# Performance work log

Measured on AMD Instinct MI355X. Metric: run time of the kernel, lower is better.

## Reference

```python
import math
import jax, jax.numpy as jnp
import numpy as np

H = 1024          # hidden size
NH = 16           # num attention heads
HD = H // NH      # head dim = 64
MAXPOS = 1024
HYP_W = 0.5


def setup_inputs() -> dict:
    key = jax.random.key(0)
    ks = jax.random.split(key, 9)
    B, S = 4, 1024
    scale = 1.0 / math.sqrt(H)
    return {
        "hidden_states": jax.random.normal(ks[0], (B, S, H), jnp.float32),
        "attention_mask": jnp.zeros((B, 1, 1, S), jnp.float32),
        "hyperbolic_attention_scores": jax.random.normal(ks[1], (B, S, S), jnp.float32),
        "Wq": jax.random.normal(ks[2], (H, H), jnp.float32) * scale,
        "bq": jnp.zeros((H,), jnp.float32),
        "Wk": jax.random.normal(ks[3], (H, H), jnp.float32) * scale,
        "bk": jnp.zeros((H,), jnp.float32),
        "Wv": jax.random.normal(ks[4], (H, H), jnp.float32) * scale,
        "bv": jnp.zeros((H,), jnp.float32),
        "dist_emb": jax.random.normal(ks[5], (2 * MAXPOS - 1, HD), jnp.float32) * 0.02,
    }


def reference(hidden_states, attention_mask, hyperbolic_attention_scores,
              Wq, bq, Wk, bk, Wv, bv, dist_emb):
    B, S, _ = hidden_states.shape

    def split_heads(x):  # [B,S,H] -> [B,NH,S,HD]
        return x.reshape(B, S, NH, HD).transpose(0, 2, 1, 3)

    q = split_heads(hidden_states @ Wq + bq)
    k = split_heads(hidden_states @ Wk + bk)
    v = split_heads(hidden_states @ Wv + bv)

    # raw scores [B,NH,Sq,Sk]
    scores = jnp.einsum("bhqd,bhkd->bhqk", q, k)

    # relative_key_query position bias
    distance = jnp.arange(S)[:, None] - jnp.arange(S)[None, :]  # [Sq,Sk]
    pe = dist_emb[distance + MAXPOS - 1]                        # [Sq,Sk,HD]
    scores = scores + jnp.einsum("bhld,lrd->bhlr", q, pe)
    scores = scores + jnp.einsum("bhrd,lrd->bhlr", k, pe)

    scores = scores / math.sqrt(HD)
    scores = scores + HYP_W * hyperbolic_attention_scores[:, None, :, :]
    scores = scores + attention_mask

    probs = jax.nn.softmax(scores, axis=-1)
    ctx = jnp.einsum("bhqk,bhkd->bhqd", probs, v)  # [B,NH,S,HD]
    ctx = ctx.transpose(0, 2, 1, 3).reshape(B, S, H)
    return ctx
```

## Files before the change

### kernel.cpp

```cpp
#include <hip/hip_runtime.h>
#include <math.h>

#define S_SEQ 1024
#define NHEAD 16
#define HDIM  64
#define BATCH 4

typedef __attribute__((ext_vector_type(8))) short bf16x8;
typedef __attribute__((ext_vector_type(4))) float f32x4;

#define MFMA16 __builtin_amdgcn_mfma_f32_16x16x32_bf16

__device__ __forceinline__ float bf2f(unsigned short h) {
    union { unsigned u; float f; } un; un.u = ((unsigned)h) << 16; return un.f;
}
__device__ __forceinline__ unsigned short f2bf(float x) {
    union { float f; unsigned u; } un; un.f = x;
    unsigned r = un.u + 0x7FFFu + ((un.u >> 16) & 1u);
    return (unsigned short)(r >> 16);
}
__device__ __forceinline__ unsigned pack2bf(float a, float b) {
    return (unsigned)f2bf(a) | ((unsigned)f2bf(b) << 16);
}
__device__ __forceinline__ void glds16(const unsigned short* g, unsigned short* l) {
    __builtin_amdgcn_global_load_lds(
        (const __attribute__((address_space(1))) void*)g,
        (__attribute__((address_space(3))) void*)l, 16, 0, 0);
}

#define HS_F4 1048576
#define PE_F4 32752
__global__ __launch_bounds__(256) void conv_kernel(
    const float* __restrict__ hs, const float* __restrict__ de,
    unsigned short* __restrict__ hsb, unsigned short* __restrict__ peb)
{
    int i = blockIdx.x * 256 + threadIdx.x;
    if (i < HS_F4) {
        float4 v = ((const float4*)hs)[i];
        uint2 o;
        o.x = pack2bf(v.x, v.y);
        o.y = pack2bf(v.z, v.w);
        *(uint2*)(hsb + 4 * (size_t)i) = o;
    } else if (i < HS_F4 + PE_F4) {
        int j = i - HS_F4;
        float4 v = ((const float4*)de)[j];
        uint2 o;
        o.x = pack2bf(v.x, v.y);
        o.y = pack2bf(v.z, v.w);
        *(uint2*)(peb + 4 * (size_t)j) = o;
    }
}

__global__ __launch_bounds__(256) void wtrans_kernel(
    const float* __restrict__ Wq, const float* __restrict__ Wk,
    const float* __restrict__ Wv, unsigned short* __restrict__ wt)
{
    __shared__ float tl[64 * 67];
    const int which = blockIdx.z;
    const float* W = (which == 0) ? Wq : (which == 1) ? Wk : Wv;
    unsigned short* out = wt + (size_t)which * 1024 * 1024;
    const int k0 = blockIdx.x * 64, n0 = blockIdx.y * 64;
    const int t = threadIdx.x;

#pragma unroll
    for (int it = 0; it < 4; ++it) {
        int idx = t + it * 256;
        int kr = idx >> 4;
        int c4 = (idx & 15) << 2;
        float4 v = *(const float4*)(W + (size_t)(k0 + kr) * 1024 + n0 + c4);
        tl[kr * 67 + c4 + 0] = v.x; tl[kr * 67 + c4 + 1] = v.y;
        tl[kr * 67 + c4 + 2] = v.z; tl[kr * 67 + c4 + 3] = v.w;
    }
    __syncthreads();
#pragma unroll
    for (int it = 0; it < 2; ++it) {
        int idx = t + it * 256;
        int nr = idx >> 3;
        int k8 = (idx & 7) << 3;
        unsigned short r[8];
#pragma unroll
        for (int e = 0; e < 8; ++e) r[e] = f2bf(tl[(k8 + e) * 67 + nr]);
        uint4 o;
        o.x = (unsigned)r[0] | ((unsigned)r[1] << 16);
        o.y = (unsigned)r[2] | ((unsigned)r[3] << 16);
        o.z = (unsigned)r[4] | ((unsigned)r[5] << 16);
        o.w = (unsigned)r[6] | ((unsigned)r[7] << 16);
        *(uint4*)(out + (size_t)(n0 + nr) * 1024 + k0 + k8) = o;
    }
}

__global__ __launch_bounds__(256, 3) void qkv_mfma_kernel(
    const unsigned short* __restrict__ hsb, const unsigned short* __restrict__ wt,
    const float* __restrict__ bq, const float* __restrict__ bk,
    const float* __restrict__ bv,
    unsigned short* __restrict__ qo, unsigned short* __restrict__ ko,
    unsigned short* __restrict__ vo)
{
    __shared__ unsigned short As[128 * 64];
    __shared__ unsigned short Bs[128 * 64];

    const int t = threadIdx.x;
    const int lane = t & 63, w = t >> 6;
    const int l16 = lane & 15, quad = lane >> 4;
    const int wm = w >> 1, wn = w & 1;
    const int lrow = lane >> 3, cs = lane & 7;
    const int n0 = blockIdx.x * 128, m0 = blockIdx.y * 128;
    const int which = blockIdx.z;
    const unsigned short* wts = wt + (size_t)which * 1024 * 1024;
    const float* bias = (which == 0) ? bq : (which == 1) ? bk : bv;

    f32x4 acc[4][4];
#pragma unroll
    for (int i = 0; i < 4; ++i)
#pragma unroll
        for (int j = 0; j < 4; ++j) acc[i][j] = (f32x4){0.f, 0.f, 0.f, 0.f};

    for (int kk = 0; kk < 1024; kk += 64) {
#pragma unroll
        for (int it = 0; it < 4; ++it) {
            int mrow = 32 * w + 8 * it + lrow;
            int kch = cs ^ (mrow & 7);
            glds16(hsb + (size_t)(m0 + mrow) * 1024 + kk + kch * 8,
                   &As[(32 * w + 8 * it) * 64]);
            glds16(wts + (size_t)(n0 + mrow) * 1024 + kk + kch * 8,
                   &Bs[(32 * w + 8 * it) * 64]);
        }
        __syncthreads();

        bf16x8 af[4][2], bf[4][2];
#pragma unroll
        for (int i = 0; i < 4; ++i) {
            int am = 64 * wm + 16 * i + l16;
            int base = am * 64;
            af[i][0] = *(bf16x8*)&As[base + ((quad ^ (am & 7)) << 3)];
            af[i][1] = *(bf16x8*)&As[base + (((quad + 4) ^ (am & 7)) << 3)];
        }
#pragma unroll
        for (int j = 0; j < 4; ++j) {
            int bn = 64 * wn + 16 * j + l16;
            int base = bn * 64;
            bf[j][0] = *(bf16x8*)&Bs[base + ((quad ^ (bn & 7)) << 3)];
            bf[j][1] = *(bf16x8*)&Bs[base + (((quad + 4) ^ (bn & 7)) << 3)];
        }
#pragma unroll
        for (int i = 0; i < 4; ++i)
#pragma unroll
            for (int j = 0; j < 4; ++j) {
                acc[i][j] = MFMA16(af[i][0], bf[j][0], acc[i][j], 0, 0, 0);
                acc[i][j] = MFMA16(af[i][1], bf[j][1], acc[i][j], 0, 0, 0);
            }
        __syncthreads();
    }

#pragma unroll
    for (int j = 0; j < 4; ++j) {
        int n = n0 + 64 * wn + 16 * j + l16;
        float bvv = bias[n];
        int hh = n >> 6, hd = n & 63;
#pragma unroll
        for (int i = 0; i < 4; ++i) {
            int mb = m0 + 64 * wm + 16 * i + 4 * quad;
            int bb = mb >> 10, s = mb & 1023;
            if (which == 2) {
                uint2 o;
                o.x = pack2bf(acc[i][j][0] + bvv, acc[i][j][1] + bvv);
                o.y = pack2bf(acc[i][j][2] + bvv, acc[i][j][3] + bvv);
                *(uint2*)(vo + ((size_t)(bb * NHEAD + hh) * HDIM + hd) * S_SEQ + s) = o;
            } else {
                unsigned short* out = (which == 0) ? qo : ko;
#pragma unroll
                for (int r = 0; r < 4; ++r)
                    out[((size_t)(bb * NHEAD + hh) * S_SEQ + s + r) * HDIM + hd] =
                        f2bf(acc[i][j][r] + bvv);
            }
        }
    }
}

__global__ __launch_bounds__(256, 4) void attn_mfma_kernel(
    const unsigned short* __restrict__ qw, const unsigned short* __restrict__ kw,
    const unsigned short* __restrict__ vtw, const unsigned short* __restrict__ peb,
    const float* __restrict__ hyp, const float* __restrict__ mask,
    float* __restrict__ out)
{
    __shared__ unsigned short pes[96 * 64];
    __shared__ unsigned short QDs[64 * 100];
    __shared__ unsigned short KDs[96 * 36];
    __shared__ unsigned short ps[64 * 32];

    const int t = threadIdx.x;
    const int lane = t & 63, w = t >> 6;
    const int l16 = lane & 15, quad = lane >> 4;
    const int lL = 16 * w + l16;
    const int l0 = blockIdx.x * 64;
    const int h = blockIdx.y, b = blockIdx.z;

    const unsigned short* qb = qw + ((size_t)(b * NHEAD + h) * S_SEQ + l0) * HDIM;
    const unsigned short* kb = kw + (size_t)(b * NHEAD + h) * S_SEQ * HDIM;
    const unsigned short* vtb = vtw + (size_t)(b * NHEAD + h) * HDIM * S_SEQ;
    const float* hypb = hyp + (size_t)b * S_SEQ * S_SEQ + (size_t)(l0 + lL) * S_SEQ;
    const float* maskb = mask + b * S_SEQ;

    const bf16x8 qf0 = *(const bf16x8*)(qb + lL * 64 + quad * 8);
    const bf16x8 qf1 = *(const bf16x8*)(qb + lL * 64 + 32 + quad * 8);

    const int pb0 = l0 + 992;
    int sb = pb0 % 96;
    int cQ = (pb0 - lL) % 96;

    const int strow = t >> 3, stp = t & 7;
    const int swzl = (lL >> 1) & 3;

    f32x4 accO[4];
#pragma unroll
    for (int jf = 0; jf < 4; ++jf) accO[jf] = (f32x4){0.f, 0.f, 0.f, 0.f};
    float m_run = -INFINITY, lsum = 0.f;

#pragma unroll
    for (int it = 0; it < 2; ++it) {
        int idx = t + it * 256;
        int row = idx >> 3, p = idx & 7;
        int ar = pb0 + 32 + row;
        int slot = ar % 96;
        int src = ar > 2046 ? 2046 : ar;
        *(uint4*)&pes[slot * 64 + (p << 3)] =
            *(const uint4*)(peb + (size_t)src * 64 + ((p ^ (slot & 7)) << 3));
    }
    __syncthreads();

#pragma unroll
    for (int jd = 0; jd < 4; ++jd) {
        int s = sb + 32 + 16 * jd + l16; if (s >= 96) s -= 96;
        const int sw = s & 7;
        bf16x8 p0 = *(bf16x8*)&pes[s * 64 + ((quad ^ sw) << 3)];
        bf16x8 p1 = *(bf16x8*)&pes[s * 64 + (((quad + 4) ^ sw) << 3)];
        f32x4 aq = (f32x4){0.f, 0.f, 0.f, 0.f};
        aq = MFMA16(p0, qf0, aq, 0, 0, 0);
        aq = MFMA16(p1, qf1, aq, 0, 0, 0);
        int cb = cQ + 32 + 16 * jd + 4 * quad;
#pragma unroll
        for (int i = 0; i < 4; ++i) {
            int c = cb + i; if (c >= 96) c -= 96;
            QDs[lL * 100 + c] = f2bf(aq[i]);
        }
    }

    bf16x8 kf00 = *(const bf16x8*)(kb + (size_t)l16 * 64 + quad * 8);
    bf16x8 kf01 = *(const bf16x8*)(kb + (size_t)l16 * 64 + 32 + quad * 8);
    bf16x8 kf10 = *(const bf16x8*)(kb + (size_t)(16 + l16) * 64 + quad * 8);
    bf16x8 kf11 = *(const bf16x8*)(kb + (size_t)(16 + l16) * 64 + 32 + quad * 8);
    uint4 peReg;
    {
        int slot = sb + strow; if (slot >= 96) slot -= 96;
        peReg = *(const uint4*)(peb + (size_t)(pb0 + strow) * 64 +
                                ((stp ^ (slot & 7)) << 3));
    }

    const int fstart = (w < 2) ? 3 * w : 2 * w + 2;
    const int fcnt   = (w < 2) ? 3 : 2;

    for (int kt = 0; kt < 32; ++kt) {
        const int r0 = 32 * kt;

        const float4 hv0 = *(const float4*)(hypb + r0 + 4 * quad);
        const float4 hv1 = *(const float4*)(hypb + r0 + 16 + 4 * quad);
        const float4 mv0 = *(const float4*)(maskb + r0 + 4 * quad);
        const float4 mv1 = *(const float4*)(maskb + r0 + 16 + 4 * quad);

        {
            int slot = sb + strow; if (slot >= 96) slot -= 96;
            *(uint4*)&pes[slot * 64 + (stp << 3)] = peReg;
        }
        __syncthreads();

        f32x4 accS0 = (f32x4){0.f, 0.f, 0.f, 0.f};
        f32x4 accS1 = (f32x4){0.f, 0.f, 0.f, 0.f};
        accS0 = MFMA16(kf00, qf0, accS0, 0, 0, 0);
        accS0 = MFMA16(kf01, qf1, accS0, 0, 0, 0);
        accS1 = MFMA16(kf10, qf0, accS1, 0, 0, 0);
        accS1 = MFMA16(kf11, qf1, accS1, 0, 0, 0);

#pragma unroll
        for (int jd = 0; jd < 2; ++jd) {
            int s = sb + 16 * jd + l16; if (s >= 96) s -= 96;
            const int sw = s & 7;
            bf16x8 p0 = *(bf16x8*)&pes[s * 64 + ((quad ^ sw) << 3)];
            bf16x8 p1 = *(bf16x8*)&pes[s * 64 + (((quad + 4) ^ sw) << 3)];
            f32x4 aq = (f32x4){0.f, 0.f, 0.f, 0.f};
            aq = MFMA16(p0, qf0, aq, 0, 0, 0);
            aq = MFMA16(p1, qf1, aq, 0, 0, 0);
            int cb = cQ + 16 * jd + 4 * quad;
#pragma unroll
            for (int i = 0; i < 4; ++i) {
                int c = cb + i; if (c >= 96) c -= 96;
                QDs[lL * 100 + c] = f2bf(aq[i]);
            }
        }

#pragma unroll
        for (int jk = 0; jk < 3; ++jk) {
            if (jk < fcnt) {
                const int f = fstart + jk;
                const int diB = 16 * ((f + 1) >> 1);
                const int rB = (f & 1) ? 0 : 16;
                int s = sb + diB + l16; if (s >= 96) s -= 96;
                const int sw = s & 7;
                bf16x8 p0 = *(bf16x8*)&pes[s * 64 + ((quad ^ sw) << 3)];
                bf16x8 p1 = *(bf16x8*)&pes[s * 64 + (((quad + 4) ^ sw) << 3)];
                f32x4 ak = (f32x4){0.f, 0.f, 0.f, 0.f};
                if (rB == 0) {
                    ak = MFMA16(p0, kf00, ak, 0, 0, 0);
                    ak = MFMA16(p1, kf01, ak, 0, 0, 0);
                } else {
                    ak = MFMA16(p0, kf10, ak, 0, 0, 0);
                    ak = MFMA16(p1, kf11, ak, 0, 0, 0);
                }
                const int colr = rB + l16;
                const int aB = diB + colr + 4 * quad - 16;
#pragma unroll
                for (int i = 0; i < 4; ++i)
                    KDs[(aB + i) * 36 + colr] = f2bf(ak[i]);
            }
        }
        __syncthreads();

        {
            const int r0n = (kt < 31) ? r0 + 32 : r0;
            kf00 = *(const bf16x8*)(kb + (size_t)(r0n + l16) * 64 + quad * 8);
            kf01 = *(const bf16x8*)(kb + (size_t)(r0n + l16) * 64 + 32 + quad * 8);
            kf10 = *(const bf16x8*)(kb + (size_t)(r0n + 16 + l16) * 64 + quad * 8);
            kf11 = *(const bf16x8*)(kb + (size_t)(r0n + 16 + l16) * 64 + 32 + quad * 8);
            int sbn = sb, pbn = pb0 - r0n;
            if (kt < 31) { sbn = sb - 32; if (sbn < 0) sbn += 96; }
            int slotN = sbn + strow; if (slotN >= 96) slotN -= 96;
            peReg = *(const uint4*)(peb + (size_t)(pbn + strow) * 64 +
                                    ((stp ^ (slotN & 7)) << 3));
        }
        bf16x8 vvA[4];
#pragma unroll
        for (int jf = 0; jf < 4; ++jf)
            vvA[jf] = *(const bf16x8*)(vtb + (size_t)(16 * jf + l16) * S_SEQ +
                                       r0 + quad * 8);

        float sc0[4], sc1[4];
        {
            uint2 qd2 = *(uint2*)&QDs[lL * 100 + sb + 28 - 4 * quad];
            uint2 kd2 = *(uint2*)&KDs[(lL + 15) * 36 + 4 * quad];
            sc0[0] = (accS0[0] + bf2f((unsigned short)(qd2.y >> 16)) +
                      bf2f((unsigned short)(kd2.x & 0xffff))) * 0.125f + 0.5f * hv0.x + mv0.x;
            sc0[1] = (accS0[1] + bf2f((unsigned short)(qd2.y & 0xffff)) +
                      bf2f((unsigned short)(kd2.x >> 16))) * 0.125f + 0.5f * hv0.y + mv0.y;
            sc0[2] = (accS0[2] + bf2f((unsigned short)(qd2.x >> 16)) +
                      bf2f((unsigned short)(kd2.y & 0xffff))) * 0.125f + 0.5f * hv0.z + mv0.z;
            sc0[3] = (accS0[3] + bf2f((unsigned short)(qd2.x & 0xffff)) +
                      bf2f((unsigned short)(kd2.y >> 16))) * 0.125f + 0.5f * hv0.w + mv0.w;
        }
        {
            uint2 qd2 = *(uint2*)&QDs[lL * 100 + sb + 12 - 4 * quad];
            uint2 kd2 = *(uint2*)&KDs[(lL + 15) * 36 + 16 + 4 * quad];
            sc1[0] = (accS1[0] + bf2f((unsigned short)(qd2.y >> 16)) +
                      bf2f((unsigned short)(kd2.x & 0xffff))) * 0.125f + 0.5f * hv1.x + mv1.x;
            sc1[1] = (accS1[1] + bf2f((unsigned short)(qd2.y & 0xffff)) +
                      bf2f((unsigned short)(kd2.x >> 16))) * 0.125f + 0.5f * hv1.y + mv1.y;
            sc1[2] = (accS1[2] + bf2f((unsigned short)(qd2.x >> 16)) +
                      bf2f((unsigned short)(kd2.y & 0xffff))) * 0.125f + 0.5f * hv1.z + mv1.z;
            sc1[3] = (accS1[3] + bf2f((unsigned short)(qd2.x & 0xffff)) +
                      bf2f((unsigned short)(kd2.y >> 16))) * 0.125f + 0.5f * hv1.w + mv1.w;
        }

        float mx = fmaxf(fmaxf(fmaxf(sc0[0], sc0[1]), fmaxf(sc0[2], sc0[3])),
                         fmaxf(fmaxf(sc1[0], sc1[1]), fmaxf(sc1[2], sc1[3])));
        mx = fmaxf(mx, __shfl_xor(mx, 16));
        mx = fmaxf(mx, __shfl_xor(mx, 32));
        const float m_new = fmaxf(m_run, mx);
        const float al = __expf(m_run - m_new);
        m_run = m_new;
        float rs = 0.f;
#pragma unroll
        for (int i = 0; i < 4; ++i) { sc0[i] = __expf(sc0[i] - m_new); rs += sc0[i]; }
#pragma unroll
        for (int i = 0; i < 4; ++i) { sc1[i] = __expf(sc1[i] - m_new); rs += sc1[i]; }
        rs += __shfl_xor(rs, 16);
        rs += __shfl_xor(rs, 32);
        lsum = lsum * al + rs;

        {
            uint2 pw;
            pw.x = pack2bf(sc0[0], sc0[1]); pw.y = pack2bf(sc0[2], sc0[3]);
            *(uint2*)&ps[lL * 32 + (((quad >> 1) ^ swzl) << 3) + 4 * (quad & 1)] = pw;
            pw.x = pack2bf(sc1[0], sc1[1]); pw.y = pack2bf(sc1[2], sc1[3]);
            *(uint2*)&ps[lL * 32 + (((2 + (quad >> 1)) ^ swzl) << 3) + 4 * (quad & 1)] = pw;
        }

        const bf16x8 pf = *(const bf16x8*)&ps[lL * 32 + ((quad ^ swzl) << 3)];
        const float alv0 = __shfl(al, 4 * quad + 0);
        const float alv1 = __shfl(al, 4 * quad + 1);
        const float alv2 = __shfl(al, 4 * quad + 2);
        const float alv3 = __shfl(al, 4 * quad + 3);
#pragma unroll
        for (int jf = 0; jf < 4; ++jf) {
            f32x4 o = accO[jf];
            o[0] *= alv0; o[1] *= alv1; o[2] *= alv2; o[3] *= alv3;
            o = MFMA16(pf, vvA[jf], o, 0, 0, 0);
            accO[jf] = o;
        }

        sb -= 32; if (sb < 0) sb += 96;
        cQ -= 32; if (cQ < 0) cQ += 96;
    }

    const float ls0 = __shfl(lsum, 4 * quad + 0);
    const float ls1 = __shfl(lsum, 4 * quad + 1);
    const float ls2 = __shfl(lsum, 4 * quad + 2);
    const float ls3 = __shfl(lsum, 4 * quad + 3);
#pragma unroll
    for (int jf = 0; jf < 4; ++jf) {
        const size_t col = (size_t)h * 64 + 16 * jf + l16;
        float* ob = out + ((size_t)b * S_SEQ + l0 + 16 * w + 4 * quad) * 1024 + col;
        ob[0]        = accO[jf][0] / ls0;
        ob[1024]     = accO[jf][1] / ls1;
        ob[2048]     = accO[jf][2] / ls2;
        ob[3072]     = accO[jf][3] / ls3;
    }
}

extern "C" void kernel_launch(void* const* d_in, const int* in_sizes, int n_in,
                              void* d_out, int out_size, void* d_ws, size_t ws_size,
                              hipStream_t stream) {
    const float* hs   = (const float*)d_in[0];
    const float* mask = (const float*)d_in[1];
    const float* hyp  = (const float*)d_in[2];
    const float* Wq   = (const float*)d_in[3];
    const float* bq   = (const float*)d_in[4];
    const float* Wk   = (const float*)d_in[5];
    const float* bk   = (const float*)d_in[6];
    const float* Wv   = (const float*)d_in[7];
    const float* bv   = (const float*)d_in[8];
    const float* de   = (const float*)d_in[9];

    char* ws = (char*)d_ws;
    unsigned short* qw  = (unsigned short*)(ws);
    unsigned short* kw  = (unsigned short*)(ws + (8u << 20));
    unsigned short* vtw = (unsigned short*)(ws + (16u << 20));
    unsigned short* hsb = (unsigned short*)(ws + (24u << 20));
    unsigned short* wt  = (unsigned short*)(ws + (32u << 20));
    unsigned short* peb = (unsigned short*)(ws + (38u << 20));

    conv_kernel<<<dim3((HS_F4 + PE_F4 + 255) / 256), 256, 0, stream>>>(hs, de, hsb, peb);
    wtrans_kernel<<<dim3(16, 16, 3), 256, 0, stream>>>(Wq, Wk, Wv, wt);
    qkv_mfma_kernel<<<dim3(8, 32, 3), 256, 0, stream>>>(hsb, wt, bq, bk, bv, qw, kw, vtw);
    attn_mfma_kernel<<<dim3(16, NHEAD, BATCH), 256, 0, stream>>>(
        qw, kw, vtw, peb, hyp, mask, (float*)d_out);
}
```

Before: 298.0 us.

## Software-pipeline K-position bias via double-buffered KDs and merge prep kernels

The attention loop now computes the key-position-bias tile for the next iteration after the PV MFMA, writing into a double-buffered KDs array, and the PE ring grows from 96 to 160 rows so the data needed ahead of time is resident. This leaves one __syncthreads per iteration instead of two, and the global loads for the next K fragments and PE row are issued at the top of the iteration. In exchange, the larger shared memory and register footprint lowers the launch bound from 4 to 3 blocks per CU. Separately, the bf16 conversion and weight-transpose kernels are merged into one launch to save a kernel launch.

```diff
diff --git a/kernel.cpp b/kernel.cpp
--- a/kernel.cpp
+++ b/kernel.cpp
@@ -30,37 +30,44 @@
 
 #define HS_F4 1048576
 #define PE_F4 32752
-__global__ __launch_bounds__(256) void conv_kernel(
+#define CONV_BLKS ((HS_F4 + PE_F4 + 255) / 256)
+
+__global__ __launch_bounds__(256) void prep_kernel(
     const float* __restrict__ hs, const float* __restrict__ de,
-    unsigned short* __restrict__ hsb, unsigned short* __restrict__ peb)
-{
-    int i = blockIdx.x * 256 + threadIdx.x;
-    if (i < HS_F4) {
-        float4 v = ((const float4*)hs)[i];
-        uint2 o;
-        o.x = pack2bf(v.x, v.y);
-        o.y = pack2bf(v.z, v.w);
-        *(uint2*)(hsb + 4 * (size_t)i) = o;
-    } else if (i < HS_F4 + PE_F4) {
-        int j = i - HS_F4;
-        float4 v = ((const float4*)de)[j];
-        uint2 o;
-        o.x = pack2bf(v.x, v.y);
-        o.y = pack2bf(v.z, v.w);
-        *(uint2*)(peb + 4 * (size_t)j) = o;
-    }
-}
-
-__global__ __launch_bounds__(256) void wtrans_kernel(
     const float* __restrict__ Wq, const float* __restrict__ Wk,
-    const float* __restrict__ Wv, unsigned short* __restrict__ wt)
+    const float* __restrict__ Wv,
+    unsigned short* __restrict__ hsb, unsigned short* __restrict__ peb,
+    unsigned short* __restrict__ wt)
 {
     __shared__ float tl[64 * 67];
-    const int which = blockIdx.z;
+    const int bx = blockIdx.x;
+    const int t = threadIdx.x;
+
+    if (bx < CONV_BLKS) {
+        int i = bx * 256 + t;
+        if (i < HS_F4) {
+            float4 v = ((const float4*)hs)[i];
+            uint2 o;
+            o.x = pack2bf(v.x, v.y);
+            o.y = pack2bf(v.z, v.w);
+            *(uint2*)(hsb + 4 * (size_t)i) = o;
+        } else if (i < HS_F4 + PE_F4) {
+            int j = i - HS_F4;
+            float4 v = ((const float4*)de)[j];
+            uint2 o;
+            o.x = pack2bf(v.x, v.y);
+            o.y = pack2bf(v.z, v.w);
+            *(uint2*)(peb + 4 * (size_t)j) = o;
+        }
+        return;
+    }
+
+    const int id = bx - CONV_BLKS;
+    const int which = id >> 8;
+    const int rem = id & 255;
     const float* W = (which == 0) ? Wq : (which == 1) ? Wk : Wv;
-    unsigned short* out = wt + (size_t)which * 1024 * 1024;
-    const int k0 = blockIdx.x * 64, n0 = blockIdx.y * 64;
-    const int t = threadIdx.x;
+    unsigned short* outp = wt + (size_t)which * 1024 * 1024;
+    const int k0 = (rem >> 4) * 64, n0 = (rem & 15) * 64;
 
 #pragma unroll
     for (int it = 0; it < 4; ++it) {
@@ -85,7 +92,7 @@
         o.y = (unsigned)r[2] | ((unsigned)r[3] << 16);
         o.z = (unsigned)r[4] | ((unsigned)r[5] << 16);
         o.w = (unsigned)r[6] | ((unsigned)r[7] << 16);
-        *(uint4*)(out + (size_t)(n0 + nr) * 1024 + k0 + k8) = o;
+        *(uint4*)(outp + (size_t)(n0 + nr) * 1024 + k0 + k8) = o;
     }
 }
 
@@ -167,25 +174,25 @@
                 o.y = pack2bf(acc[i][j][2] + bvv, acc[i][j][3] + bvv);
                 *(uint2*)(vo + ((size_t)(bb * NHEAD + hh) * HDIM + hd) * S_SEQ + s) = o;
             } else {
-                unsigned short* out = (which == 0) ? qo : ko;
+                unsigned short* outp = (which == 0) ? qo : ko;
 #pragma unroll
                 for (int r = 0; r < 4; ++r)
-                    out[((size_t)(bb * NHEAD + hh) * S_SEQ + s + r) * HDIM + hd] =
+                    outp[((size_t)(bb * NHEAD + hh) * S_SEQ + s + r) * HDIM + hd] =
                         f2bf(acc[i][j][r] + bvv);
             }
         }
     }
 }
 
-__global__ __launch_bounds__(256, 4) void attn_mfma_kernel(
+__global__ __launch_bounds__(256, 3) void attn_mfma_kernel(
     const unsigned short* __restrict__ qw, const unsigned short* __restrict__ kw,
     const unsigned short* __restrict__ vtw, const unsigned short* __restrict__ peb,
     const float* __restrict__ hyp, const float* __restrict__ mask,
     float* __restrict__ out)
 {
-    __shared__ unsigned short pes[96 * 64];
+    __shared__ unsigned short pes[160 * 64];
     __shared__ unsigned short QDs[64 * 100];
-    __shared__ unsigned short KDs[96 * 36];
+    __shared__ unsigned short KDs[2][96 * 36];
     __shared__ unsigned short ps[64 * 32];
 
     const int t = threadIdx.x;
@@ -205,23 +212,37 @@
     const bf16x8 qf1 = *(const bf16x8*)(qb + lL * 64 + 32 + quad * 8);
 
     const int pb0 = l0 + 992;
-    int sb = pb0 % 96;
+    int sbP = pb0 % 160;
+    int sbQ = pb0 % 96;
     int cQ = (pb0 - lL) % 96;
 
     const int strow = t >> 3, stp = t & 7;
     const int swzl = (lL >> 1) & 3;
 
+    const int fstart = (w < 2) ? 3 * w : 2 * w + 2;
+    const int fcnt   = (w < 2) ? 3 : 2;
+
     f32x4 accO[4];
 #pragma unroll
     for (int jf = 0; jf < 4; ++jf) accO[jf] = (f32x4){0.f, 0.f, 0.f, 0.f};
     float m_run = -INFINITY, lsum = 0.f;
 
-#pragma unroll
-    for (int it = 0; it < 2; ++it) {
+    bf16x8 kfC0 = *(const bf16x8*)(kb + (size_t)l16 * 64 + quad * 8);
+    bf16x8 kfC1 = *(const bf16x8*)(kb + (size_t)l16 * 64 + 32 + quad * 8);
+    bf16x8 kfC2 = *(const bf16x8*)(kb + (size_t)(16 + l16) * 64 + quad * 8);
+    bf16x8 kfC3 = *(const bf16x8*)(kb + (size_t)(16 + l16) * 64 + 32 + quad * 8);
+    uint4 peReg;
+    {
+        int ar = pb0 - 64 + strow;
+        peReg = *(const uint4*)(peb + (size_t)ar * 64 + ((stp ^ (ar & 7)) << 3));
+    }
+
+#pragma unroll
+    for (int it = 0; it < 4; ++it) {
         int idx = t + it * 256;
         int row = idx >> 3, p = idx & 7;
-        int ar = pb0 + 32 + row;
-        int slot = ar % 96;
+        int ar = pb0 - 32 + row;
+        int slot = ar % 160;
         int src = ar > 2046 ? 2046 : ar;
         *(uint4*)&pes[slot * 64 + (p << 3)] =
             *(const uint4*)(peb + (size_t)src * 64 + ((p ^ (slot & 7)) << 3));
@@ -230,7 +251,7 @@
 
 #pragma unroll
     for (int jd = 0; jd < 4; ++jd) {
-        int s = sb + 32 + 16 * jd + l16; if (s >= 96) s -= 96;
+        int s = sbP + 32 + 16 * jd + l16; if (s >= 160) s -= 160;
         const int sw = s & 7;
         bf16x8 p0 = *(bf16x8*)&pes[s * 64 + ((quad ^ sw) << 3)];
         bf16x8 p1 = *(bf16x8*)&pes[s * 64 + (((quad + 4) ^ sw) << 3)];
@@ -245,44 +266,76 @@
         }
     }
 
-    bf16x8 kf00 = *(const bf16x8*)(kb + (size_t)l16 * 64 + quad * 8);
-    bf16x8 kf01 = *(const bf16x8*)(kb + (size_t)l16 * 64 + 32 + quad * 8);
-    bf16x8 kf10 = *(const bf16x8*)(kb + (size_t)(16 + l16) * 64 + quad * 8);
-    bf16x8 kf11 = *(const bf16x8*)(kb + (size_t)(16 + l16) * 64 + 32 + quad * 8);
-    uint4 peReg;
     {
-        int slot = sb + strow; if (slot >= 96) slot -= 96;
-        peReg = *(const uint4*)(peb + (size_t)(pb0 + strow) * 64 +
-                                ((stp ^ (slot & 7)) << 3));
-    }
-
-    const int fstart = (w < 2) ? 3 * w : 2 * w + 2;
-    const int fcnt   = (w < 2) ? 3 : 2;
+        unsigned short* kdp = KDs[0];
+#pragma unroll
+        for (int jk = 0; jk < 3; ++jk) {
+            if (jk < fcnt) {
+                const int f = fstart + jk;
+                const int diB = 16 * ((f + 1) >> 1);
+                const int rB = (f & 1) ? 0 : 16;
+                int s = sbP + diB + l16; if (s >= 160) s -= 160;
+                const int sw = s & 7;
+                bf16x8 p0 = *(bf16x8*)&pes[s * 64 + ((quad ^ sw) << 3)];
+                bf16x8 p1 = *(bf16x8*)&pes[s * 64 + (((quad + 4) ^ sw) << 3)];
+                f32x4 ak = (f32x4){0.f, 0.f, 0.f, 0.f};
+                if (rB == 0) {
+                    ak = MFMA16(p0, kfC0, ak, 0, 0, 0);
+                    ak = MFMA16(p1, kfC1, ak, 0, 0, 0);
+                } else {
+                    ak = MFMA16(p0, kfC2, ak, 0, 0, 0);
+                    ak = MFMA16(p1, kfC3, ak, 0, 0, 0);
+                }
+                const int colr = rB + l16;
+                const int aB = diB + colr + 4 * quad - 16;
+#pragma unroll
+                for (int i = 0; i < 4; ++i)
+                    kdp[(aB + i) * 36 + colr] = f2bf(ak[i]);
+            }
+        }
+    }
 
     for (int kt = 0; kt < 32; ++kt) {
         const int r0 = 32 * kt;
+        __syncthreads();
 
         const float4 hv0 = *(const float4*)(hypb + r0 + 4 * quad);
         const float4 hv1 = *(const float4*)(hypb + r0 + 16 + 4 * quad);
         const float4 mv0 = *(const float4*)(maskb + r0 + 4 * quad);
         const float4 mv1 = *(const float4*)(maskb + r0 + 16 + 4 * quad);
-
+        bf16x8 vvA[4];
+#pragma unroll
+        for (int jf = 0; jf < 4; ++jf)
+            vvA[jf] = *(const bf16x8*)(vtb + (size_t)(16 * jf + l16) * S_SEQ +
+                                       r0 + quad * 8);
+        const int r0n = (kt < 31) ? r0 + 32 : r0;
+        bf16x8 kfN0 = *(const bf16x8*)(kb + (size_t)(r0n + l16) * 64 + quad * 8);
+        bf16x8 kfN1 = *(const bf16x8*)(kb + (size_t)(r0n + l16) * 64 + 32 + quad * 8);
+        bf16x8 kfN2 = *(const bf16x8*)(kb + (size_t)(r0n + 16 + l16) * 64 + quad * 8);
+        bf16x8 kfN3 = *(const bf16x8*)(kb + (size_t)(r0n + 16 + l16) * 64 + 32 + quad * 8);
+        uint4 peRegN;
         {
-            int slot = sb + strow; if (slot >= 96) slot -= 96;
+            int ar = pb0 - r0 - 96 + strow;
+            int src = ar < 0 ? 0 : ar;
+            peRegN = *(const uint4*)(peb + (size_t)src * 64 + ((stp ^ (ar & 7)) << 3));
+        }
+
+        {
+            int sbS = sbP - 64; if (sbS < 0) sbS += 160;
+            int slot = sbS + strow; if (slot >= 160) slot -= 160;
             *(uint4*)&pes[slot * 64 + (stp << 3)] = peReg;
         }
-        __syncthreads();
 
         f32x4 accS0 = (f32x4){0.f, 0.f, 0.f, 0.f};
         f32x4 accS1 = (f32x4){0.f, 0.f, 0.f, 0.f};
-        accS0 = MFMA16(kf00, qf0, accS0, 0, 0, 0);
-        accS0 = MFMA16(kf01, qf1, accS0, 0, 0, 0);
-        accS1 = MFMA16(kf10, qf0, accS1, 0, 0, 0);
-        accS1 = MFMA16(kf11, qf1, accS1, 0, 0, 0);
+        accS0 = MFMA16(kfC0, qf0, accS0, 0, 0, 0);
+        accS0 = MFMA16(kfC1, qf1, accS0, 0, 0, 0);
+        accS1 = MFMA16(kfC2, qf0, accS1, 0, 0, 0);
+        accS1 = MFMA16(kfC3, qf1, accS1, 0, 0, 0);
 
 #pragma unroll
         for (int jd = 0; jd < 2; ++jd) {
-            int s = sb + 16 * jd + l16; if (s >= 96) s -= 96;
+            int s = sbP + 16 * jd + l16; if (s >= 160) s -= 160;
             const int sw = s & 7;
             bf16x8 p0 = *(bf16x8*)&pes[s * 64 + ((quad ^ sw) << 3)];
             bf16x8 p1 = *(bf16x8*)&pes[s * 64 + (((quad + 4) ^ sw) << 3)];
@@ -297,55 +350,11 @@
             }
         }
 
-#pragma unroll
-        for (int jk = 0; jk < 3; ++jk) {
-            if (jk < fcnt) {
-                const int f = fstart + jk;
-                const int diB = 16 * ((f + 1) >> 1);
-                const int rB = (f & 1) ? 0 : 16;
-                int s = sb + diB + l16; if (s >= 96) s -= 96;
-                const int sw = s & 7;
-                bf16x8 p0 = *(bf16x8*)&pes[s * 64 + ((quad ^ sw) << 3)];
-                bf16x8 p1 = *(bf16x8*)&pes[s * 64 + (((quad + 4) ^ sw) << 3)];
-                f32x4 ak = (f32x4){0.f, 0.f, 0.f, 0.f};
-                if (rB == 0) {
-                    ak = MFMA16(p0, kf00, ak, 0, 0, 0);
-                    ak = MFMA16(p1, kf01, ak, 0, 0, 0);
-                } else {
-                    ak = MFMA16(p0, kf10, ak, 0, 0, 0);
-                    ak = MFMA16(p1, kf11, ak, 0, 0, 0);
-                }
-                const int colr = rB + l16;
-                const int aB = diB + colr + 4 * quad - 16;
-#pragma unroll
-                for (int i = 0; i < 4; ++i)
-                    KDs[(aB + i) * 36 + colr] = f2bf(ak[i]);
-            }
-        }
-        __syncthreads();
-
-        {
-            const int r0n = (kt < 31) ? r0 + 32 : r0;
-            kf00 = *(const bf16x8*)(kb + (size_t)(r0n + l16) * 64 + quad * 8);
-            kf01 = *(const bf16x8*)(kb + (size_t)(r0n + l16) * 64 + 32 + quad * 8);
-            kf10 = *(const bf16x8*)(kb + (size_t)(r0n + 16 + l16) * 64 + quad * 8);
-            kf11 = *(const bf16x8*)(kb + (size_t)(r0n + 16 + l16) * 64 + 32 + quad * 8);
-            int sbn = sb, pbn = pb0 - r0n;
-            if (kt < 31) { sbn = sb - 32; if (sbn < 0) sbn += 96; }
-            int slotN = sbn + strow; if (slotN >= 96) slotN -= 96;
-            peReg = *(const uint4*)(peb + (size_t)(pbn + strow) * 64 +
-                                    ((stp ^ (slotN & 7)) << 3));
-        }
-        bf16x8 vvA[4];
-#pragma unroll
-        for (int jf = 0; jf < 4; ++jf)
-            vvA[jf] = *(const bf16x8*)(vtb + (size_t)(16 * jf + l16) * S_SEQ +
-                                       r0 + quad * 8);
-
+        const unsigned short* kdc = KDs[kt & 1];
         float sc0[4], sc1[4];
         {
-            uint2 qd2 = *(uint2*)&QDs[lL * 100 + sb + 28 - 4 * quad];
-            uint2 kd2 = *(uint2*)&KDs[(lL + 15) * 36 + 4 * quad];
+            uint2 qd2 = *(uint2*)&QDs[lL * 100 + sbQ + 28 - 4 * quad];
+            uint2 kd2 = *(uint2*)&kdc[(lL + 15) * 36 + 4 * quad];
             sc0[0] = (accS0[0] + bf2f((unsigned short)(qd2.y >> 16)) +
                       bf2f((unsigned short)(kd2.x & 0xffff))) * 0.125f + 0.5f * hv0.x + mv0.x;
             sc0[1] = (accS0[1] + bf2f((unsigned short)(qd2.y & 0xffff)) +
@@ -356,8 +365,8 @@
                       bf2f((unsigned short)(kd2.y >> 16))) * 0.125f + 0.5f * hv0.w + mv0.w;
         }
         {
-            uint2 qd2 = *(uint2*)&QDs[lL * 100 + sb + 12 - 4 * quad];
-            uint2 kd2 = *(uint2*)&KDs[(lL + 15) * 36 + 16 + 4 * quad];
+            uint2 qd2 = *(uint2*)&QDs[lL * 100 + sbQ + 12 - 4 * quad];
+            uint2 kd2 = *(uint2*)&kdc[(lL + 15) * 36 + 16 + 4 * quad];
             sc1[0] = (accS1[0] + bf2f((unsigned short)(qd2.y >> 16)) +
                       bf2f((unsigned short)(kd2.x & 0xffff))) * 0.125f + 0.5f * hv1.x + mv1.x;
             sc1[1] = (accS1[1] + bf2f((unsigned short)(qd2.y & 0xffff)) +
@@ -405,7 +414,40 @@
             accO[jf] = o;
         }
 
-        sb -= 32; if (sb < 0) sb += 96;
+        if (kt < 31) {
+            unsigned short* kdp = KDs[(kt + 1) & 1];
+            int sW = sbP - 32; if (sW < 0) sW += 160;
+#pragma unroll
+            for (int jk = 0; jk < 3; ++jk) {
+                if (jk < fcnt) {
+                    const int f = fstart + jk;
+                    const int diB = 16 * ((f + 1) >> 1);
+                    const int rB = (f & 1) ? 0 : 16;
+                    int s = sW + diB + l16; if (s >= 160) s -= 160;
+                    const int sw = s & 7;
+                    bf16x8 p0 = *(bf16x8*)&pes[s * 64 + ((quad ^ sw) << 3)];
+                    bf16x8 p1 = *(bf16x8*)&pes[s * 64 + (((quad + 4) ^ sw) << 3)];
+                    f32x4 ak = (f32x4){0.f, 0.f, 0.f, 0.f};
+                    if (rB == 0) {
+                        ak = MFMA16(p0, kfN0, ak, 0, 0, 0);
+                        ak = MFMA16(p1, kfN1, ak, 0, 0, 0);
+                    } else {
+                        ak = MFMA16(p0, kfN2, ak, 0, 0, 0);
+                        ak = MFMA16(p1, kfN3, ak, 0, 0, 0);
+                    }
+                    const int colr = rB + l16;
+                    const int aB = diB + colr + 4 * quad - 16;
+#pragma unroll
+                    for (int i = 0; i < 4; ++i)
+                        kdp[(aB + i) * 36 + colr] = f2bf(ak[i]);
+                }
+            }
+        }
+
+        kfC0 = kfN0; kfC1 = kfN1; kfC2 = kfN2; kfC3 = kfN3;
+        peReg = peRegN;
+        sbP -= 32; if (sbP < 0) sbP += 160;
+        sbQ -= 32; if (sbQ < 0) sbQ += 96;
         cQ -= 32; if (cQ < 0) cQ += 96;
     }
 
@@ -446,8 +488,8 @@
     unsigned short* wt  = (unsigned short*)(ws + (32u << 20));
     unsigned short* peb = (unsigned short*)(ws + (38u << 20));
 
-    conv_kernel<<<dim3((HS_F4 + PE_F4 + 255) / 256), 256, 0, stream>>>(hs, de, hsb, peb);
-    wtrans_kernel<<<dim3(16, 16, 3), 256, 0, stream>>>(Wq, Wk, Wv, wt);
+    prep_kernel<<<dim3(CONV_BLKS + 768), 256, 0, stream>>>(hs, de, Wq, Wk, Wv,
+                                                           hsb, peb, wt);
     qkv_mfma_kernel<<<dim3(8, 32, 3), 256, 0, stream>>>(hsb, wt, bq, bk, bv, qw, kw, vtw);
     attn_mfma_kernel<<<dim3(16, NHEAD, BATCH), 256, 0, stream>>>(
         qw, kw, vtw, peb, hyp, mask, (float*)d_out);
```

Result: slower. 321.8 us (+8.0%).
